# Optimization experiments

Hardware: AMD Instinct MI355X
Metric: run time of the kernel (lower is better)

## Reference

```python
import jax, jax.numpy as jnp
import numpy as np

# Cell hyperparameters (from model.cell / Eprop_fit.__init__)
THRESHOLD = 0.6
DAMPENING = 0.3
N_REF = 5
DECAY = 0.8          # membrane decay used for pre-synaptic trace filters
ELIG_DECAY = 0.8     # default decay in exp_convolve for eligibility filtering
REG = 300.0


def exp_convolve(t, decay):
    """Causal exponential filter along time axis 1: a_t = decay*a_{t-1} + x_t."""
    xt = jnp.moveaxis(t, 1, 0)  # time-major [T, B, ...]

    def step(acc, cur):
        acc = acc * decay + cur
        return acc, acc

    _, y = jax.lax.scan(step, jnp.zeros_like(xt[0]), xt)
    return jnp.moveaxis(y, 0, 1)


def refractory_count(z, n_ref):
    """ref_count[t] depends on z[:t]; starts at 0."""
    zt = jnp.moveaxis(jax.lax.stop_gradient(z), 1, 0)  # [T, B, N]
    init = jnp.zeros(zt.shape[1:], jnp.int32)

    def step(c, zc):
        c = jnp.where(zc > 0, jnp.int32(n_ref - 1), jnp.maximum(0, c - 1))
        return c, c

    _, counts = jax.lax.scan(step, init, zt[:-1])
    counts = jnp.concatenate([init[None], counts], axis=0)
    return jnp.moveaxis(counts, 0, 1)  # [B, T, N]


def setup_inputs() -> dict:
    key = jax.random.key(0)
    k1, k2, k3, k4, k5, k6 = jax.random.split(key, 6)
    B, T, N, NIN, K = 4, 300, 200, 100, 10
    v = jax.random.normal(k1, (B, T, N), jnp.float32) * 0.5 + 0.3
    z = (jax.random.uniform(k2, (B, T, N)) < 0.05).astype(jnp.float32)  # spikes
    x = (jax.random.uniform(k3, (B, T, NIN)) < 0.1).astype(jnp.float32)
    error1 = jax.random.normal(k4, (B, T, K), jnp.float32) * 0.1   # output error
    error2 = jax.random.normal(k5, (N,), jnp.float32) * 0.01       # firing-rate error
    w_out = jax.random.normal(k6, (N, K), jnp.float32) / np.sqrt(N)
    return {"v": v, "z": z, "x": x, "error1": error1, "error2": error2, "w_out": w_out}


def reference(v, z, x, error1, error2, w_out):
    B, T, N = v.shape

    v_scaled = (v - THRESHOLD) / THRESHOLD
    psi_no_ref = DAMPENING * jnp.maximum(1.0 - jnp.abs(v_scaled), 0.0) / THRESHOLD

    ref = refractory_count(z, N_REF)
    post_term = jnp.where(ref > 0, 0.0, psi_no_ref)  # [B, T, N]

    # shift z by one time step (z_{t-1}, zero-initialized)
    z_prev = jnp.concatenate([jnp.zeros_like(z[:, :1]), z[:, :-1]], axis=1)

    pre_w_in = exp_convolve(x, DECAY)        # x_bar  [B, T, n_in]
    pre_w_rec = exp_convolve(z_prev, DECAY)  # z_bar  [B, T, N]
    pre_w_out = exp_convolve(z, DECAY)       # [B, T, N]

    # eligibility traces: [B, T, pre, post]
    et_in = post_term[:, :, None, :] * pre_w_in[:, :, :, None]
    et_rec = post_term[:, :, None, :] * pre_w_rec[:, :, :, None]

    fet_in = exp_convolve(et_in, ELIG_DECAY)
    fet_rec = exp_convolve(et_rec, ELIG_DECAY)

    avg_in = jnp.mean(et_in, axis=(0, 1))    # [n_in, N]
    avg_rec = jnp.mean(et_rec, axis=(0, 1))  # [N, N]

    # learning signals (symmetric e-prop): L = error @ w_out^T
    learning_signals = jnp.einsum('btk,jk->btj', error1, w_out)  # [B, T, N]

    dloss_dw_out = jnp.einsum('btk,btj->jk', error1, pre_w_out)          # [N, K]
    dloss_dw_in = jnp.einsum('btj,btij->ij', learning_signals, fet_in)   # [n_in, N]
    dloss_dw_rec = jnp.einsum('btj,btij->ij', learning_signals, fet_rec) # [N, N]

    dloss_dw_in = dloss_dw_in + REG * (error2 * avg_in)
    dloss_dw_rec = dloss_dw_rec + REG * (error2 * avg_rec)

    # mask autapses (diagonal of recurrent weight gradient)
    eye = jnp.eye(N, dtype=bool)
    dloss_dw_rec = jnp.where(eye, 0.0, dloss_dw_rec)

    return dloss_dw_in, dloss_dw_rec, dloss_dw_out
```

## Files before the change

### kernel.cpp

```cpp
#include <hip/hip_runtime.h>

#define BB    4
#define TT    300
#define NN    200
#define NINN  100
#define KK    10
#define DECAY 0.8f
#define THR   0.6f
#define DAMP  0.3f

#define LCH   20
#define NCHK  (TT / LCH)
#define WARM  48

#define XBAR_OFF  0
#define ZFILT_OFF (BB*TT*NINN)
#define ZBAR_OFF  (ZFILT_OFF + BB*TT*NN)
#define CBUF_OFF  (ZBAR_OFF  + BB*TT*NN)
#define GBAR_OFF  (CBUF_OFF  + BB*TT*NN)

#define R_A_N     (BB*NCHK*NINN)
#define R_B_BASE  6144
#define R_B_N     (BB*NCHK*NN)
#define R_G_BASE  18176
#define R_G_N     (BB*NCHK*KK)
#define R_Z_BASE  18944
#define R_Z_N     500
#define K1_TOTAL  (R_Z_BASE + R_Z_N)

__global__ void scan_kernel(const float* __restrict__ z,
                            const float* __restrict__ x,
                            const float* __restrict__ error1,
                            float* __restrict__ ws,
                            float* __restrict__ out) {
    int tid = blockIdx.x * blockDim.x + threadIdx.x;
    float* xbar  = ws + XBAR_OFF;
    float* zfilt = ws + ZFILT_OFF;
    float* zbar  = ws + ZBAR_OFF;
    float* gbar  = ws + GBAR_OFF;

    if (tid < R_A_N) {
        int i = tid % NINN, r = tid / NINN;
        int chunk = r % NCHK, b = r / NCHK;
        int t0 = chunk * LCH;
        const float* src = x + (size_t)b * TT * NINN + i;
        float acc = 0.f;
        #pragma unroll
        for (int d = WARM; d >= 1; --d) {
            int t = t0 - d;
            int tc = t < 0 ? 0 : t;
            float val = src[tc * NINN];
            acc = DECAY * acc + (t < 0 ? 0.f : val);
        }
        float vals[LCH];
        #pragma unroll
        for (int tt = 0; tt < LCH; ++tt) vals[tt] = src[(t0 + tt) * NINN];
        #pragma unroll
        for (int tt = 0; tt < LCH; ++tt) { acc = DECAY * acc + vals[tt]; vals[tt] = acc; }
        float* dst = xbar + (size_t)b * TT * NINN + i;
        #pragma unroll
        for (int tt = 0; tt < LCH; ++tt) dst[(t0 + tt) * NINN] = vals[tt];
    } else if (tid >= R_B_BASE && tid < R_B_BASE + R_B_N) {
        int u = tid - R_B_BASE;
        int j = u % NN, r = u / NN;
        int chunk = r % NCHK, b = r / NCHK;
        int t0 = chunk * LCH;
        const float* src = z + (size_t)b * TT * NN + j;
        float acc = 0.f;
        #pragma unroll
        for (int d = WARM; d >= 1; --d) {
            int t = t0 - d;
            int tc = t < 0 ? 0 : t;
            float val = src[tc * NN];
            acc = DECAY * acc + (t < 0 ? 0.f : val);
        }
        float zv[LCH], pre[LCH];
        #pragma unroll
        for (int tt = 0; tt < LCH; ++tt) zv[tt] = src[(t0 + tt) * NN];
        #pragma unroll
        for (int tt = 0; tt < LCH; ++tt) {
            pre[tt] = acc;
            acc = DECAY * acc + zv[tt];
            zv[tt] = acc;
        }
        float* dzb = zbar  + (size_t)b * TT * NN + j;
        float* dzf = zfilt + (size_t)b * TT * NN + j;
        #pragma unroll
        for (int tt = 0; tt < LCH; ++tt) dzb[(t0 + tt) * NN] = pre[tt];
        #pragma unroll
        for (int tt = 0; tt < LCH; ++tt) dzf[(t0 + tt) * NN] = zv[tt];
    } else if (tid >= R_G_BASE && tid < R_G_BASE + R_G_N) {
        int u = tid - R_G_BASE;
        int k = u % KK, r = u / KK;
        int chunk = r % NCHK, b = r / NCHK;
        int t0 = chunk * LCH, t1 = t0 + LCH - 1;
        const float* src = error1 + (size_t)b * TT * KK + k;
        float G = 0.f;
        #pragma unroll
        for (int d = WARM; d >= 1; --d) {
            int t = t1 + d;
            int tc = t > TT - 1 ? TT - 1 : t;
            float val = src[tc * KK];
            G = DECAY * G + (t > TT - 1 ? 0.f : val);
        }
        float ev[LCH];
        #pragma unroll
        for (int tt = 0; tt < LCH; ++tt) ev[tt] = src[(t1 - tt) * KK];
        float* dst = gbar + (size_t)b * TT * KK + k;
        #pragma unroll
        for (int tt = 0; tt < LCH; ++tt) {
            G = DECAY * G + ev[tt];
            dst[(t1 - tt) * KK] = G;
        }
    } else if (tid >= R_Z_BASE && tid < R_Z_BASE + R_Z_N) {
        int u = tid - R_Z_BASE;
        ((float4*)(out + NINN * NN + NN * NN))[u] = make_float4(0.f, 0.f, 0.f, 0.f);
    }
}

__global__ void c_kernel(const float* __restrict__ v,
                         const float* __restrict__ z,
                         const float* __restrict__ error2,
                         const float* __restrict__ w_out,
                         float* __restrict__ ws) {
    int tid = blockIdx.x * blockDim.x + threadIdx.x;
    if (tid >= BB * TT * NN) return;
    const float* gbar = ws + GBAR_OFF;
    float* cbuf = ws + CBUF_OFF;

    int j = tid % NN, bt = tid / NN;
    int t = bt % TT, b = bt / TT;

    float Ldot = 0.f;
    #pragma unroll
    for (int k = 0; k < KK; ++k)
        Ldot += gbar[bt * KK + k] * w_out[j * KK + k];
    float coeff = 0.25f * error2[j];

    bool refr = false;
    #pragma unroll
    for (int d = 1; d <= 4; ++d) {
        int s = t - d;
        int sc = s < 0 ? 0 : s;
        float zv = z[(b * TT + sc) * NN + j];
        if (s >= 0 && zv > 0.f) refr = true;
    }
    float vv = v[bt * NN + j];
    float vs = (vv - THR) / THR;
    float psi = (DAMP / THR) * fmaxf(1.f - fabsf(vs), 0.f);
    cbuf[bt * NN + j] = (refr ? 0.f : psi) * (Ldot + coeff);
}

#define SKB 16
#define KC3 (BB * TT / SKB)
#define PT  4
#define JT  64

__global__ void out_kernel(const float* __restrict__ error1,
                           const float* __restrict__ ws,
                           float* __restrict__ out) {
    __shared__ float red[SKB * PT * JT];
    int bid = blockIdx.x;
    int tid = threadIdx.x;
    const float* xbar  = ws + XBAR_OFF;
    const float* zfilt = ws + ZFILT_OFF;
    const float* zbar  = ws + ZBAR_OFF;
    const float* cbuf  = ws + CBUF_OFF;

    if (bid < 300) {
        int pt = bid >> 2;
        int jt = bid & 3;
        int p0 = pt * PT;
        int j0 = jt * JT;
        int W = NN - j0; if (W > JT) W = JT;
        int jq = tid & 15;
        int s  = tid >> 4;

        if (jq * 4 < W) {
            bool isrec = (p0 >= NINN);
            const float* A = isrec ? (zbar + (p0 - NINN)) : (xbar + p0);
            int lda = isrec ? NN : NINN;
            const float* C = cbuf + j0 + jq * 4;
            int bt0 = s * KC3;
            float acc[4][4];
            #pragma unroll
            for (int a = 0; a < 4; ++a)
                #pragma unroll
                for (int c = 0; c < 4; ++c) acc[a][c] = 0.f;
            #pragma unroll 5
            for (int rr = 0; rr < KC3; ++rr) {
                int bt = bt0 + rr;
                float4 av = *(const float4*)(A + (size_t)bt * lda);
                float4 cv = *(const float4*)(C + (size_t)bt * NN);
                float am[4] = {av.x, av.y, av.z, av.w};
                float cm[4] = {cv.x, cv.y, cv.z, cv.w};
                #pragma unroll
                for (int a = 0; a < 4; ++a)
                    #pragma unroll
                    for (int c = 0; c < 4; ++c) acc[a][c] += am[a] * cm[c];
            }
            float* dst = red + s * (PT * JT) + jq * 4;
            #pragma unroll
            for (int a = 0; a < 4; ++a)
                *(float4*)(dst + a * JT) =
                    make_float4(acc[a][0], acc[a][1], acc[a][2], acc[a][3]);
        }
        __syncthreads();

        int o = tid;
        int pl = o >> 6, jl = o & 63;
        if (jl < W) {
            float sum = 0.f;
            #pragma unroll
            for (int s2 = 0; s2 < SKB; ++s2) sum += red[s2 * (PT * JT) + o];
            int row = p0 + pl;
            int j = j0 + jl;
            if (row < NINN) {
                out[row * NN + j] = sum;
            } else {
                int i = row - NINN;
                out[NINN * NN + i * NN + j] = (i == j) ? 0.f : sum;
            }
        }
    } else {
        int u = (bid - 300) * 256 + tid;
        if (u < 6 * NN * KK) {
            int jk = u % (NN * KK);
            int s = u / (NN * KK);
            int j = jk % NN;
            int k = jk / NN;
            int bt0 = s * 200;
            float acc = 0.f;
            #pragma unroll 8
            for (int rr = 0; rr < 200; ++rr) {
                int bt = bt0 + rr;
                acc += zfilt[bt * NN + j] * error1[bt * KK + k];
            }
            atomicAdd(out + NINN * NN + NN * NN + j * KK + k, acc);
        }
    }
}

extern "C" void kernel_launch(void* const* d_in, const int* in_sizes, int n_in,
                              void* d_out, int out_size, void* d_ws, size_t ws_size,
                              hipStream_t stream) {
    const float* v  = (const float*)d_in[0];
    const float* z  = (const float*)d_in[1];
    const float* x  = (const float*)d_in[2];
    const float* e1 = (const float*)d_in[3];
    const float* e2 = (const float*)d_in[4];
    const float* wo = (const float*)d_in[5];
    float* out = (float*)d_out;
    float* ws  = (float*)d_ws;

    scan_kernel<<<(K1_TOTAL + 255) / 256, 256, 0, stream>>>(z, x, e1, ws, out);

    c_kernel<<<(BB * TT * NN + 255) / 256, 256, 0, stream>>>(v, z, e2, wo, ws);

    out_kernel<<<347, 256, 0, stream>>>(e1, ws, out);
}
```

Baseline: 87.48 us.

## Fuse learning-signal coefficient computation into scan kernel, dropping separate c_kernel

Moves the per-(b,t,j) coefficient computation into the scan kernel as a new thread range. Each thread there runs the backward-filtered error scan for all K outputs over its time chunk, with warm-up, and combines it with w_out, the refractory window and the surrogate derivative. This removes one kernel launch and the gbar workspace round trip. In exchange each thread redundantly recomputes the K-wide error filter, including the 48-step warm-up, so there is more ALU work and more repeated error1 loads.

After: 181.9 us. 2.08x slower.

```diff
diff --git a/kernel.cpp b/kernel.cpp
--- a/kernel.cpp
+++ b/kernel.cpp
@@ -17,27 +17,29 @@
 #define ZFILT_OFF (BB*TT*NINN)
 #define ZBAR_OFF  (ZFILT_OFF + BB*TT*NN)
 #define CBUF_OFF  (ZBAR_OFF  + BB*TT*NN)
-#define GBAR_OFF  (CBUF_OFF  + BB*TT*NN)
 
 #define R_A_N     (BB*NCHK*NINN)
 #define R_B_BASE  6144
 #define R_B_N     (BB*NCHK*NN)
-#define R_G_BASE  18176
-#define R_G_N     (BB*NCHK*KK)
-#define R_Z_BASE  18944
+#define R_C_BASE  18176
+#define R_C_N     (BB*NCHK*NN)
+#define R_Z_BASE  30208
 #define R_Z_N     500
 #define K1_TOTAL  (R_Z_BASE + R_Z_N)
 
-__global__ void scan_kernel(const float* __restrict__ z,
+__global__ void scan_kernel(const float* __restrict__ v,
+                            const float* __restrict__ z,
                             const float* __restrict__ x,
                             const float* __restrict__ error1,
+                            const float* __restrict__ error2,
+                            const float* __restrict__ w_out,
                             float* __restrict__ ws,
                             float* __restrict__ out) {
     int tid = blockIdx.x * blockDim.x + threadIdx.x;
     float* xbar  = ws + XBAR_OFF;
     float* zfilt = ws + ZFILT_OFF;
     float* zbar  = ws + ZBAR_OFF;
-    float* gbar  = ws + GBAR_OFF;
+    float* cbuf  = ws + CBUF_OFF;
 
     if (tid < R_A_N) {
         int i = tid % NINN, r = tid / NINN;
@@ -89,66 +91,70 @@
         for (int tt = 0; tt < LCH; ++tt) dzb[(t0 + tt) * NN] = pre[tt];
         #pragma unroll
         for (int tt = 0; tt < LCH; ++tt) dzf[(t0 + tt) * NN] = zv[tt];
-    } else if (tid >= R_G_BASE && tid < R_G_BASE + R_G_N) {
-        int u = tid - R_G_BASE;
-        int k = u % KK, r = u / KK;
+    } else if (tid >= R_C_BASE && tid < R_C_BASE + R_C_N) {
+        int u = tid - R_C_BASE;
+        int j = u % NN, r = u / NN;
         int chunk = r % NCHK, b = r / NCHK;
         int t0 = chunk * LCH, t1 = t0 + LCH - 1;
-        const float* src = error1 + (size_t)b * TT * KK + k;
-        float G = 0.f;
+
+        float wj[KK];
+        #pragma unroll
+        for (int k = 0; k < KK; ++k) wj[k] = w_out[j * KK + k];
+        float coeff = 0.25f * error2[j];
+
+        float Gk[KK];
+        #pragma unroll
+        for (int k = 0; k < KK; ++k) Gk[k] = 0.f;
         #pragma unroll
         for (int d = WARM; d >= 1; --d) {
             int t = t1 + d;
             int tc = t > TT - 1 ? TT - 1 : t;
-            float val = src[tc * KK];
-            G = DECAY * G + (t > TT - 1 ? 0.f : val);
-        }
-        float ev[LCH];
-        #pragma unroll
-        for (int tt = 0; tt < LCH; ++tt) ev[tt] = src[(t1 - tt) * KK];
-        float* dst = gbar + (size_t)b * TT * KK + k;
-        #pragma unroll
-        for (int tt = 0; tt < LCH; ++tt) {
-            G = DECAY * G + ev[tt];
-            dst[(t1 - tt) * KK] = G;
+            const float* e = error1 + ((size_t)b * TT + tc) * KK;
+            bool oob = (t > TT - 1);
+            #pragma unroll
+            for (int h = 0; h < KK / 2; ++h) {
+                float2 ev = *(const float2*)(e + 2 * h);
+                Gk[2 * h]     = DECAY * Gk[2 * h]     + (oob ? 0.f : ev.x);
+                Gk[2 * h + 1] = DECAY * Gk[2 * h + 1] + (oob ? 0.f : ev.y);
+            }
+        }
+
+        float zwin[LCH + 4];
+        #pragma unroll
+        for (int q = 0; q < LCH + 4; ++q) {
+            int s = t0 - 4 + q;
+            int sc = s < 0 ? 0 : s;
+            float zl = z[((size_t)b * TT + sc) * NN + j];
+            zwin[q] = (s < 0) ? 0.f : zl;
+        }
+        float vv[LCH];
+        #pragma unroll
+        for (int tt = 0; tt < LCH; ++tt)
+            vv[tt] = v[((size_t)b * TT + t0 + tt) * NN + j];
+
+        #pragma unroll
+        for (int tt = LCH - 1; tt >= 0; --tt) {
+            int t = t0 + tt;
+            const float* e = error1 + ((size_t)b * TT + t) * KK;
+            #pragma unroll
+            for (int h = 0; h < KK / 2; ++h) {
+                float2 ev = *(const float2*)(e + 2 * h);
+                Gk[2 * h]     = DECAY * Gk[2 * h]     + ev.x;
+                Gk[2 * h + 1] = DECAY * Gk[2 * h + 1] + ev.y;
+            }
+            float L = 0.f;
+            #pragma unroll
+            for (int k = 0; k < KK; ++k) L += wj[k] * Gk[k];
+            bool refr = (zwin[tt] > 0.f) || (zwin[tt + 1] > 0.f) ||
+                        (zwin[tt + 2] > 0.f) || (zwin[tt + 3] > 0.f);
+            float vs = (vv[tt] - THR) / THR;
+            float psi = (DAMP / THR) * fmaxf(1.f - fabsf(vs), 0.f);
+            cbuf[((size_t)b * TT + t) * NN + j] = (refr ? 0.f : psi) * (L + coeff);
         }
     } else if (tid >= R_Z_BASE && tid < R_Z_BASE + R_Z_N) {
         int u = tid - R_Z_BASE;
         ((float4*)(out + NINN * NN + NN * NN))[u] = make_float4(0.f, 0.f, 0.f, 0.f);
     }
-}
-
-__global__ void c_kernel(const float* __restrict__ v,
-                         const float* __restrict__ z,
-                         const float* __restrict__ error2,
-                         const float* __restrict__ w_out,
-                         float* __restrict__ ws) {
-    int tid = blockIdx.x * blockDim.x + threadIdx.x;
-    if (tid >= BB * TT * NN) return;
-    const float* gbar = ws + GBAR_OFF;
-    float* cbuf = ws + CBUF_OFF;
-
-    int j = tid % NN, bt = tid / NN;
-    int t = bt % TT, b = bt / TT;
-
-    float Ldot = 0.f;
-    #pragma unroll
-    for (int k = 0; k < KK; ++k)
-        Ldot += gbar[bt * KK + k] * w_out[j * KK + k];
-    float coeff = 0.25f * error2[j];
-
-    bool refr = false;
-    #pragma unroll
-    for (int d = 1; d <= 4; ++d) {
-        int s = t - d;
-        int sc = s < 0 ? 0 : s;
-        float zv = z[(b * TT + sc) * NN + j];
-        if (s >= 0 && zv > 0.f) refr = true;
-    }
-    float vv = v[bt * NN + j];
-    float vs = (vv - THR) / THR;
-    float psi = (DAMP / THR) * fmaxf(1.f - fabsf(vs), 0.f);
-    cbuf[bt * NN + j] = (refr ? 0.f : psi) * (Ldot + coeff);
 }
 
 #define SKB 16
@@ -253,9 +259,8 @@
     float* out = (float*)d_out;
     float* ws  = (float*)d_ws;
 
-    scan_kernel<<<(K1_TOTAL + 255) / 256, 256, 0, stream>>>(z, x, e1, ws, out);
-
-    c_kernel<<<(BB * TT * NN + 255) / 256, 256, 0, stream>>>(v, z, e2, wo, ws);
+    scan_kernel<<<(K1_TOTAL + 255) / 256, 256, 0, stream>>>(
+        v, z, x, e1, e2, wo, ws, out);
 
     out_kernel<<<347, 256, 0, stream>>>(e1, ws, out);
 }
```
